# Kernel optimization log

Measured on AMD Instinct MI355X. Metric: run time of the kernel, lower is better.

Reference implementation:

```python
import jax, jax.numpy as jnp
import numpy as np

B, D, H, O = 4096, 1024, 8192, 1000

def _l2norm_rows(w):
    return w / jnp.maximum(jnp.linalg.norm(w, axis=1, keepdims=True), 1e-12)

def setup_inputs() -> dict:
    key = jax.random.key(0)
    k1, k2, k3 = jax.random.split(key, 3)
    x = jax.random.normal(k1, (B, D), dtype=jnp.float32)
    kohonen_weights = _l2norm_rows(jax.random.normal(k2, (H, D), dtype=jnp.float32))
    grossberg_weights = _l2norm_rows(jax.random.normal(k3, (O, H), dtype=jnp.float32))
    return {"x": x, "kohonen_weights": kohonen_weights, "grossberg_weights": grossberg_weights}

def reference(x, kohonen_weights, grossberg_weights):
    # x: [B, D] (already flat), kohonen_weights: [H, D], grossberg_weights: [O, H]
    x2 = jnp.sum(x * x, axis=1, keepdims=True)              # [B, 1]
    w2 = jnp.sum(kohonen_weights * kohonen_weights, axis=1)  # [H]
    # Euclidean cdist via the expanded quadratic form (same as torch.cdist p=2)
    sq = x2 + w2[None, :] - 2.0 * (x @ kohonen_weights.T)    # [B, H]
    distances = jnp.sqrt(jnp.maximum(sq, 0.0))
    winners = jnp.argmin(distances, axis=1)                  # [B] int
    # one_hot @ grossberg_weights.T is exactly a row gather of grossberg_weights.T
    output = jnp.take(grossberg_weights.T, winners, axis=0)  # [B, O]
    return (output, winners)
```

## Files before the change

kernel.cpp:

```cpp
#include <hip/hip_runtime.h>
#include <hip/hip_bf16.h>
#include <hip/hip_fp16.h>


#define BB 4096
#define DD 1024
#define HH 8192
#define OO 1000

#define BM 128
#define BN 128
#define BK 64
#define NTILES (HH / BN)

typedef _Float16 f16;
typedef _Float16 f16x4 __attribute__((ext_vector_type(4)));
typedef _Float16 f16x8 __attribute__((ext_vector_type(8)));
typedef float f32x4 __attribute__((ext_vector_type(4)));

typedef __attribute__((address_space(3))) uint32_t lds_u32_t;
typedef __attribute__((address_space(1))) uint32_t glb_u32_t;

__device__ __forceinline__ uint32_t packkey(float v, int col) {
  uint32_t u = __float_as_uint(v);
  uint32_t mask = (uint32_t)((int32_t)u >> 31) | 0x80000000u;
  u ^= mask;
  return (u & 0xFFFFFF80u) | (uint32_t)col;
}
__device__ __forceinline__ float unpackval(uint32_t k) {
  uint32_t u = k & 0xFFFFFF80u;
  uint32_t mask = (k & 0x80000000u) ? 0x80000000u : 0xFFFFFFFFu;
  return __uint_as_float(u ^ mask);
}

__device__ __forceinline__ void kmerge(uint32_t& k1, uint32_t& k2,
                                       uint32_t o1, uint32_t o2) {
  uint32_t mn = min(k1, o1);
  uint32_t alt = (k1 > o1) ? k2 : o2;
  k1 = max(k1, o1);
  k2 = max(mn, alt);
}

__global__ __launch_bounds__(256) void cvt_kernel(
    const float* __restrict__ x, const float* __restrict__ kw,
    f16* __restrict__ xh, f16* __restrict__ kh,
    const float* __restrict__ G, float* __restrict__ Gt) {
  const int blk = blockIdx.x;
  const int tid = threadIdx.x;
  __shared__ float tile[32][33];
  if (blk < BB + HH) {
    const float* src = (blk < BB) ? (x + (size_t)blk * DD)
                                  : (kw + (size_t)(blk - BB) * DD);
    f16* dst = (blk < BB) ? (xh + (size_t)blk * DD)
                          : (kh + (size_t)(blk - BB) * DD);
    float4 v = ((const float4*)src)[tid];
    f16x4 h;
    h[0] = (f16)v.x; h[1] = (f16)v.y; h[2] = (f16)v.z; h[3] = (f16)v.w;
    *(f16x4*)(dst + 4 * tid) = h;
  } else {
    const int tile_id = blk - (BB + HH);
    const int h0 = (tile_id >> 5) * 32;
    const int o0 = (tile_id & 31) * 32;
    const int tx = tid & 31;
    const int ty = tid >> 5;
#pragma unroll
    for (int j = 0; j < 4; ++j) {
      int o = o0 + ty + j * 8;
      if (o < OO) tile[ty + j * 8][tx] = G[(size_t)o * HH + h0 + tx];
    }
    __syncthreads();
#pragma unroll
    for (int j = 0; j < 4; ++j) {
      int o = o0 + tx;
      int h = h0 + ty + j * 8;
      if (o < OO) Gt[(size_t)h * OO + o] = tile[tx][ty + j * 8];
    }
  }
}

__global__ __launch_bounds__(256) void gemm_top2(
    const f16* __restrict__ A, const f16* __restrict__ Bt,
    uint2* __restrict__ pk) {
  __shared__ __align__(16) f16 sA[BM * BK];
  __shared__ __align__(16) f16 sB[BN * BK];
  __shared__ uint2 mk[128][2];

  const int tid = threadIdx.x;
  const int w = tid >> 6;
  const int L = tid & 63;
  const int m0 = blockIdx.y * BM;
  const int n0 = blockIdx.x * BN;
  const int rm = (w >> 1) * 64;
  const int cn = (w & 1) * 64;

  f32x4 acc[4][4];
#pragma unroll
  for (int i = 0; i < 4; ++i)
#pragma unroll
    for (int j = 0; j < 4; ++j) {
      acc[i][j][0] = 0.f; acc[i][j][1] = 0.f; acc[i][j][2] = 0.f; acc[i][j][3] = 0.f;
    }

  const int lm = L & 15;
  const int lq = L >> 4;

  const int r0 = tid >> 3;
  const int sc0 = ((tid & 7) ^ (r0 & 7)) * 8;
  const f16* pA = A + (size_t)(m0 + r0) * DD + sc0;
  const f16* pB = Bt + (size_t)(n0 + r0) * DD + sc0;
  const size_t rstep = (size_t)32 * DD;

  const int swz = (lm & 7);
  const int ra0 = (rm + lm) * BK + ((0 * 4 + lq) ^ swz) * 8;
  const int ra1 = (rm + lm) * BK + ((1 * 4 + lq) ^ swz) * 8;
  const int rb0 = (cn + lm) * BK + ((0 * 4 + lq) ^ swz) * 8;
  const int rb1 = (cn + lm) * BK + ((1 * 4 + lq) ^ swz) * 8;

  for (int kt = 0; kt < DD / BK; ++kt) {
    __syncthreads();
#pragma unroll
    for (int j = 0; j < 4; ++j) {
      __builtin_amdgcn_global_load_lds((const glb_u32_t*)(pA + j * rstep),
                                       (lds_u32_t*)(sA + (tid + j * 256) * 8), 16, 0, 0);
      __builtin_amdgcn_global_load_lds((const glb_u32_t*)(pB + j * rstep),
                                       (lds_u32_t*)(sB + (tid + j * 256) * 8), 16, 0, 0);
    }
    pA += BK; pB += BK;
    __syncthreads();

    f16x8 af[4], bf[4];
#pragma unroll
    for (int i = 0; i < 4; ++i)
      af[i] = *(const f16x8*)(sA + ra0 + i * 16 * BK);
#pragma unroll
    for (int j = 0; j < 4; ++j)
      bf[j] = *(const f16x8*)(sB + rb0 + j * 16 * BK);
#pragma unroll
    for (int i = 0; i < 4; ++i)
#pragma unroll
      for (int j = 0; j < 4; ++j)
        acc[i][j] = __builtin_amdgcn_mfma_f32_16x16x32_f16(af[i], bf[j], acc[i][j], 0, 0, 0);
#pragma unroll
    for (int i = 0; i < 4; ++i)
      af[i] = *(const f16x8*)(sA + ra1 + i * 16 * BK);
#pragma unroll
    for (int j = 0; j < 4; ++j)
      bf[j] = *(const f16x8*)(sB + rb1 + j * 16 * BK);
#pragma unroll
    for (int i = 0; i < 4; ++i)
#pragma unroll
      for (int j = 0; j < 4; ++j)
        acc[i][j] = __builtin_amdgcn_mfma_f32_16x16x32_f16(af[i], bf[j], acc[i][j], 0, 0, 0);
  }

  const int col0 = cn + lm;
#pragma unroll
  for (int i = 0; i < 4; ++i) {
#pragma unroll
    for (int r = 0; r < 4; ++r) {
      uint32_t k1 = 0, k2 = 0;
#pragma unroll
      for (int j = 0; j < 4; ++j) {
        uint32_t kj = packkey(acc[i][j][r], col0 + j * 16);
        if (kj > k1) { k2 = k1; k1 = kj; }
        else k2 = max(k2, kj);
      }
#pragma unroll
      for (int msk = 1; msk < 16; msk <<= 1) {
        uint32_t o1 = (uint32_t)__shfl_xor((int)k1, msk, 64);
        uint32_t o2 = (uint32_t)__shfl_xor((int)k2, msk, 64);
        kmerge(k1, k2, o1, o2);
      }
      if (lm == 0) {
        int rl = rm + i * 16 + lq * 4 + r;
        mk[rl][w & 1] = make_uint2(k1, k2);
      }
    }
  }
  __syncthreads();
  if (tid < 128) {
    uint2 a = mk[tid][0], b = mk[tid][1];
    kmerge(a.x, a.y, b.x, b.y);
    pk[(size_t)(m0 + tid) * NTILES + blockIdx.x] = a;
  }
}

__global__ __launch_bounds__(256) void select_kernel(
    const float* __restrict__ x, const float* __restrict__ kw,
    const uint2* __restrict__ pk,
    const float* __restrict__ Gt, float* __restrict__ out,
    float* __restrict__ out_w, int* __restrict__ winners) {
  const int b = blockIdx.x * 4 + (threadIdx.x >> 6);
  const int L = threadIdx.x & 63;

  const float4* x4 = (const float4*)(x + (size_t)b * DD);
  float4 xv[4];
#pragma unroll
  for (int j = 0; j < 4; ++j) xv[j] = x4[L + 64 * j];

  uint2 kp = pk[(size_t)b * NTILES + L];

  double x2 = 0.0;
#pragma unroll
  for (int j = 0; j < 4; ++j)
    x2 += (double)xv[j].x * xv[j].x + (double)xv[j].y * xv[j].y +
          (double)xv[j].z * xv[j].z + (double)xv[j].w * xv[j].w;
#pragma unroll
  for (int msk = 1; msk < 64; msk <<= 1) x2 += __shfl_xor(x2, msk, 64);

  uint32_t m = kp.x;
#pragma unroll
  for (int msk = 1; msk < 64; msk <<= 1)
    m = max(m, (uint32_t)__shfl_xor((int)m, msk, 64));
  const uint32_t thrk = packkey(unpackval(m) - 0.01f, 0);

  unsigned long long cand1 = __ballot(kp.x >= thrk);
  unsigned long long cand2 = __ballot(kp.y >= thrk);

  double best = 1e300;
  int bestc = 0x7fffffff;
#pragma unroll 1
  for (int pass = 0; pass < 2; ++pass) {
    unsigned long long bits = (pass == 0) ? cand1 : cand2;
    uint32_t mykey = (pass == 0) ? kp.x : kp.y;
    while (bits) {
      int t = __ffsll((long long)bits) - 1;
      bits &= bits - 1;
      uint32_t kbt = (uint32_t)__shfl((int)mykey, t, 64);
      int col = t * 128 + (int)(kbt & 127u);
      const float4* k4 = (const float4*)(kw + (size_t)col * DD);
      double dot = 0.0, w2 = 0.0;
#pragma unroll
      for (int j = 0; j < 4; ++j) {
        float4 wv = k4[L + 64 * j];
        dot += (double)xv[j].x * wv.x + (double)xv[j].y * wv.y +
               (double)xv[j].z * wv.z + (double)xv[j].w * wv.w;
        w2 += (double)wv.x * wv.x + (double)wv.y * wv.y +
              (double)wv.z * wv.z + (double)wv.w * wv.w;
      }
#pragma unroll
      for (int msk = 1; msk < 64; msk <<= 1) {
        dot += __shfl_xor(dot, msk, 64);
        w2 += __shfl_xor(w2, msk, 64);
      }
      double sq = x2 + w2 - 2.0 * dot;
      if (sq < best || (sq == best && col < bestc)) { best = sq; bestc = col; }
    }
  }

  if (L == 0) {
    out_w[b] = (float)bestc;
    winners[b] = bestc;
  }
  if (Gt != nullptr) {
    const float4* gsrc = (const float4*)(Gt + (size_t)bestc * OO);
    float4* gdst = (float4*)(out + (size_t)b * OO);
#pragma unroll
    for (int j = 0; j < 4; ++j) {
      int q = L + 64 * j;
      if (q < OO / 4) gdst[q] = gsrc[q];
    }
  }
}

__global__ __launch_bounds__(256) void gather_kernel(
    const float* __restrict__ G, const int* __restrict__ winners,
    float* __restrict__ out) {
  const int b = blockIdx.y;
  const int o = blockIdx.x * 256 + threadIdx.x;
  if (o < OO) {
    int w = winners[b];
    out[(size_t)b * OO + o] = G[(size_t)o * HH + w];
  }
}

extern "C" void kernel_launch(void* const* d_in, const int* in_sizes, int n_in,
                              void* d_out, int out_size, void* d_ws, size_t ws_size,
                              hipStream_t stream) {
  const float* x  = (const float*)d_in[0];
  const float* kw = (const float*)d_in[1];
  const float* gw = (const float*)d_in[2];
  float* out = (float*)d_out;

  const size_t MB = 1024 * 1024;
  char* ws = (char*)d_ws;
  f16*    xh      = (f16*)(ws);
  f16*    kh      = (f16*)(ws + 8 * MB);
  uint2*  pk      = (uint2*)(ws + 24 * MB);
  int*    winners = (int*)(ws + 26 * MB);
  float*  Gt      = (float*)(ws + 26 * MB + 65536);
  const size_t need = 26 * MB + 65536 + sizeof(float) * (size_t)HH * OO;
  const bool use_transpose = ws_size >= need;

  int cvt_blocks = BB + HH + (use_transpose ? 8192 : 0);
  cvt_kernel<<<cvt_blocks, 256, 0, stream>>>(x, kw, xh, kh, gw,
                                             use_transpose ? Gt : nullptr);

  dim3 g(HH / BN, BB / BM);
  gemm_top2<<<g, 256, 0, stream>>>(xh, kh, pk);

  select_kernel<<<BB / 4, 256, 0, stream>>>(x, kw, pk,
                                            use_transpose ? Gt : nullptr,
                                            out, out + (size_t)BB * OO, winners);

  if (!use_transpose) {
    gather_kernel<<<dim3((OO + 255) / 256, BB), 256, 0, stream>>>(gw, winners, out);
  }
}
```

Measured before the change: 226.0 us.

## Fuse convert, GEMM-top2 and select into one cooperative persistent kernel

Replaces the three separate launches (convert/transpose, GEMM with top-2 keys, select+gather) with a single cooperative kernel of 1024 persistent blocks that loops over the work and uses grid-wide syncs between phases. Each block handles two GEMM tiles and four select rows. The aim is to remove launch gaps and kernel boundary overheads. In exchange it adds grid.sync costs and caps occupancy at 4 blocks per CU. If the cooperative launch fails, it falls back to the multi-kernel path.

```diff
diff --git a/kernel.cpp b/kernel.cpp
--- a/kernel.cpp
+++ b/kernel.cpp
@@ -1,6 +1,9 @@
 #include <hip/hip_runtime.h>
 #include <hip/hip_bf16.h>
 #include <hip/hip_fp16.h>
+#include <hip/hip_cooperative_groups.h>
+
+namespace cg = cooperative_groups;
 
 
 #define BB 4096
@@ -12,6 +15,7 @@
 #define BN 128
 #define BK 64
 #define NTILES (HH / BN)
+#define GRID_BLKS 1024
 
 typedef _Float16 f16;
 typedef _Float16 f16x4 __attribute__((ext_vector_type(4)));
@@ -32,13 +36,270 @@
   uint32_t mask = (k & 0x80000000u) ? 0x80000000u : 0xFFFFFFFFu;
   return __uint_as_float(u ^ mask);
 }
-
 __device__ __forceinline__ void kmerge(uint32_t& k1, uint32_t& k2,
                                        uint32_t o1, uint32_t o2) {
   uint32_t mn = min(k1, o1);
   uint32_t alt = (k1 > o1) ? k2 : o2;
   k1 = max(k1, o1);
   k2 = max(mn, alt);
+}
+
+
+__device__ __forceinline__ void convert_row(const float* __restrict__ src,
+                                            f16* __restrict__ dst, int tid) {
+  float4 v = ((const float4*)src)[tid];
+  f16x4 h;
+  h[0] = (f16)v.x; h[1] = (f16)v.y; h[2] = (f16)v.z; h[3] = (f16)v.w;
+  *(f16x4*)(dst + 4 * tid) = h;
+}
+
+__device__ __forceinline__ void transpose_tile(const float* __restrict__ G,
+                                               float* __restrict__ Gt,
+                                               float (*tile)[33],
+                                               int tile_id, int tid) {
+  const int h0 = (tile_id >> 5) * 32;
+  const int o0 = (tile_id & 31) * 32;
+  const int tx = tid & 31;
+  const int ty = tid >> 5;
+  __syncthreads();
+#pragma unroll
+  for (int j = 0; j < 4; ++j) {
+    int o = o0 + ty + j * 8;
+    if (o < OO) tile[ty + j * 8][tx] = G[(size_t)o * HH + h0 + tx];
+  }
+  __syncthreads();
+#pragma unroll
+  for (int j = 0; j < 4; ++j) {
+    int o = o0 + tx;
+    int h = h0 + ty + j * 8;
+    if (o < OO) Gt[(size_t)h * OO + o] = tile[tx][ty + j * 8];
+  }
+}
+
+__device__ __forceinline__ void gemm_tile(const f16* __restrict__ A,
+                                          const f16* __restrict__ Bt,
+                                          uint2* __restrict__ pk,
+                                          f16* sA, f16* sB, uint2 (*mk)[2],
+                                          int bx, int by, int tid) {
+  const int w = tid >> 6;
+  const int L = tid & 63;
+  const int m0 = by * BM;
+  const int n0 = bx * BN;
+  const int rm = (w >> 1) * 64;
+  const int cn = (w & 1) * 64;
+
+  f32x4 acc[4][4];
+#pragma unroll
+  for (int i = 0; i < 4; ++i)
+#pragma unroll
+    for (int j = 0; j < 4; ++j) {
+      acc[i][j][0] = 0.f; acc[i][j][1] = 0.f; acc[i][j][2] = 0.f; acc[i][j][3] = 0.f;
+    }
+
+  const int lm = L & 15;
+  const int lq = L >> 4;
+
+  const int r0 = tid >> 3;
+  const int sc0 = ((tid & 7) ^ (r0 & 7)) * 8;
+  const f16* pA = A + (size_t)(m0 + r0) * DD + sc0;
+  const f16* pB = Bt + (size_t)(n0 + r0) * DD + sc0;
+  const size_t rstep = (size_t)32 * DD;
+
+  const int swz = (lm & 7);
+  const int ra0 = (rm + lm) * BK + ((0 * 4 + lq) ^ swz) * 8;
+  const int ra1 = (rm + lm) * BK + ((1 * 4 + lq) ^ swz) * 8;
+  const int rb0 = (cn + lm) * BK + ((0 * 4 + lq) ^ swz) * 8;
+  const int rb1 = (cn + lm) * BK + ((1 * 4 + lq) ^ swz) * 8;
+
+  for (int kt = 0; kt < DD / BK; ++kt) {
+    __syncthreads();
+#pragma unroll
+    for (int j = 0; j < 4; ++j) {
+      __builtin_amdgcn_global_load_lds((const glb_u32_t*)(pA + j * rstep),
+                                       (lds_u32_t*)(sA + (tid + j * 256) * 8), 16, 0, 0);
+      __builtin_amdgcn_global_load_lds((const glb_u32_t*)(pB + j * rstep),
+                                       (lds_u32_t*)(sB + (tid + j * 256) * 8), 16, 0, 0);
+    }
+    pA += BK; pB += BK;
+    __syncthreads();
+
+    f16x8 af[4], bf[4];
+#pragma unroll
+    for (int i = 0; i < 4; ++i)
+      af[i] = *(const f16x8*)(sA + ra0 + i * 16 * BK);
+#pragma unroll
+    for (int j = 0; j < 4; ++j)
+      bf[j] = *(const f16x8*)(sB + rb0 + j * 16 * BK);
+#pragma unroll
+    for (int i = 0; i < 4; ++i)
+#pragma unroll
+      for (int j = 0; j < 4; ++j)
+        acc[i][j] = __builtin_amdgcn_mfma_f32_16x16x32_f16(af[i], bf[j], acc[i][j], 0, 0, 0);
+#pragma unroll
+    for (int i = 0; i < 4; ++i)
+      af[i] = *(const f16x8*)(sA + ra1 + i * 16 * BK);
+#pragma unroll
+    for (int j = 0; j < 4; ++j)
+      bf[j] = *(const f16x8*)(sB + rb1 + j * 16 * BK);
+#pragma unroll
+    for (int i = 0; i < 4; ++i)
+#pragma unroll
+      for (int j = 0; j < 4; ++j)
+        acc[i][j] = __builtin_amdgcn_mfma_f32_16x16x32_f16(af[i], bf[j], acc[i][j], 0, 0, 0);
+  }
+
+  const int col0 = cn + lm;
+#pragma unroll
+  for (int i = 0; i < 4; ++i) {
+#pragma unroll
+    for (int r = 0; r < 4; ++r) {
+      uint32_t k1 = 0, k2 = 0;
+#pragma unroll
+      for (int j = 0; j < 4; ++j) {
+        uint32_t kj = packkey(acc[i][j][r], col0 + j * 16);
+        if (kj > k1) { k2 = k1; k1 = kj; }
+        else k2 = max(k2, kj);
+      }
+#pragma unroll
+      for (int msk = 1; msk < 16; msk <<= 1) {
+        uint32_t o1 = (uint32_t)__shfl_xor((int)k1, msk, 64);
+        uint32_t o2 = (uint32_t)__shfl_xor((int)k2, msk, 64);
+        kmerge(k1, k2, o1, o2);
+      }
+      if (lm == 0) {
+        int rl = rm + i * 16 + lq * 4 + r;
+        mk[rl][w & 1] = make_uint2(k1, k2);
+      }
+    }
+  }
+  __syncthreads();
+  if (tid < 128) {
+    uint2 a = mk[tid][0], b = mk[tid][1];
+    kmerge(a.x, a.y, b.x, b.y);
+    pk[(size_t)(m0 + tid) * NTILES + bx] = a;
+  }
+  __syncthreads();
+}
+
+__device__ __forceinline__ void select_row(const float* __restrict__ x,
+                                           const float* __restrict__ kw,
+                                           const uint2* __restrict__ pk,
+                                           const float* __restrict__ Gt,
+                                           const float* __restrict__ G,
+                                           float* __restrict__ out,
+                                           float* __restrict__ out_w,
+                                           int b, int L) {
+  const float4* x4 = (const float4*)(x + (size_t)b * DD);
+  float4 xv[4];
+#pragma unroll
+  for (int j = 0; j < 4; ++j) xv[j] = x4[L + 64 * j];
+
+  uint2 kp = pk[(size_t)b * NTILES + L];
+
+  double x2 = 0.0;
+#pragma unroll
+  for (int j = 0; j < 4; ++j)
+    x2 += (double)xv[j].x * xv[j].x + (double)xv[j].y * xv[j].y +
+          (double)xv[j].z * xv[j].z + (double)xv[j].w * xv[j].w;
+#pragma unroll
+  for (int msk = 1; msk < 64; msk <<= 1) x2 += __shfl_xor(x2, msk, 64);
+
+  uint32_t m = kp.x;
+#pragma unroll
+  for (int msk = 1; msk < 64; msk <<= 1)
+    m = max(m, (uint32_t)__shfl_xor((int)m, msk, 64));
+  const uint32_t thrk = packkey(unpackval(m) - 0.01f, 0);
+
+  unsigned long long cand1 = __ballot(kp.x >= thrk);
+  unsigned long long cand2 = __ballot(kp.y >= thrk);
+
+  double best = 1e300;
+  int bestc = 0x7fffffff;
+#pragma unroll 1
+  for (int pass = 0; pass < 2; ++pass) {
+    unsigned long long bits = (pass == 0) ? cand1 : cand2;
+    uint32_t mykey = (pass == 0) ? kp.x : kp.y;
+    while (bits) {
+      int t = __ffsll((long long)bits) - 1;
+      bits &= bits - 1;
+      uint32_t kbt = (uint32_t)__shfl((int)mykey, t, 64);
+      int col = t * 128 + (int)(kbt & 127u);
+      const float4* k4 = (const float4*)(kw + (size_t)col * DD);
+      double dot = 0.0, w2 = 0.0;
+#pragma unroll
+      for (int j = 0; j < 4; ++j) {
+        float4 wv = k4[L + 64 * j];
+        dot += (double)xv[j].x * wv.x + (double)xv[j].y * wv.y +
+               (double)xv[j].z * wv.z + (double)xv[j].w * wv.w;
+        w2 += (double)wv.x * wv.x + (double)wv.y * wv.y +
+              (double)wv.z * wv.z + (double)wv.w * wv.w;
+      }
+#pragma unroll
+      for (int msk = 1; msk < 64; msk <<= 1) {
+        dot += __shfl_xor(dot, msk, 64);
+        w2 += __shfl_xor(w2, msk, 64);
+      }
+      double sq = x2 + w2 - 2.0 * dot;
+      if (sq < best || (sq == best && col < bestc)) { best = sq; bestc = col; }
+    }
+  }
+
+  if (L == 0) out_w[b] = (float)bestc;
+  if (Gt != nullptr) {
+    const float4* gsrc = (const float4*)(Gt + (size_t)bestc * OO);
+    float4* gdst = (float4*)(out + (size_t)b * OO);
+#pragma unroll
+    for (int j = 0; j < 4; ++j) {
+      int q = L + 64 * j;
+      if (q < OO / 4) gdst[q] = gsrc[q];
+    }
+  } else {
+#pragma unroll 1
+    for (int j = 0; j < 16; ++j) {
+      int o = L + 64 * j;
+      if (o < OO) out[(size_t)b * OO + o] = G[(size_t)o * HH + bestc];
+    }
+  }
+}
+
+__global__ __launch_bounds__(256, 4) void mega_kernel(
+    const float* __restrict__ x, const float* __restrict__ kw,
+    const float* __restrict__ G,
+    f16* __restrict__ xh, f16* __restrict__ kh, float* __restrict__ Gt,
+    uint2* __restrict__ pk, float* __restrict__ out, float* __restrict__ out_w) {
+  __shared__ __align__(16) char smem[34816];
+  f16* sA = (f16*)smem;
+  f16* sB = (f16*)(smem + 16384);
+  uint2 (*mk)[2] = (uint2(*)[2])(smem + 32768);
+  float (*ttile)[33] = (float(*)[33])smem;
+
+  const int bid = blockIdx.x;
+  const int tid = threadIdx.x;
+  cg::grid_group grid = cg::this_grid();
+
+#pragma unroll 1
+  for (int r = bid; r < BB + HH; r += GRID_BLKS) {
+    const float* src = (r < BB) ? (x + (size_t)r * DD) : (kw + (size_t)(r - BB) * DD);
+    f16* dst = (r < BB) ? (xh + (size_t)r * DD) : (kh + (size_t)(r - BB) * DD);
+    convert_row(src, dst, tid);
+  }
+  if (Gt != nullptr) {
+#pragma unroll 1
+    for (int t = bid; t < 8192; t += GRID_BLKS)
+      transpose_tile(G, Gt, ttile, t, tid);
+  }
+  __threadfence();
+  grid.sync();
+
+#pragma unroll 1
+  for (int tt = 0; tt < 2; ++tt) {
+    int t = bid + tt * GRID_BLKS;
+    gemm_tile(xh, kh, pk, sA, sB, mk, t & 63, t >> 6, tid);
+  }
+  __threadfence();
+  grid.sync();
+
+  select_row(x, kw, pk, Gt, G, out, out_w, bid * 4 + (tid >> 6), tid & 63);
 }
 
 __global__ __launch_bounds__(256) void cvt_kernel(
@@ -53,28 +314,9 @@
                                   : (kw + (size_t)(blk - BB) * DD);
     f16* dst = (blk < BB) ? (xh + (size_t)blk * DD)
                           : (kh + (size_t)(blk - BB) * DD);
-    float4 v = ((const float4*)src)[tid];
-    f16x4 h;
-    h[0] = (f16)v.x; h[1] = (f16)v.y; h[2] = (f16)v.z; h[3] = (f16)v.w;
-    *(f16x4*)(dst + 4 * tid) = h;
+    convert_row(src, dst, tid);
   } else {
-    const int tile_id = blk - (BB + HH);
-    const int h0 = (tile_id >> 5) * 32;
-    const int o0 = (tile_id & 31) * 32;
-    const int tx = tid & 31;
-    const int ty = tid >> 5;
-#pragma unroll
-    for (int j = 0; j < 4; ++j) {
-      int o = o0 + ty + j * 8;
-      if (o < OO) tile[ty + j * 8][tx] = G[(size_t)o * HH + h0 + tx];
-    }
-    __syncthreads();
-#pragma unroll
-    for (int j = 0; j < 4; ++j) {
-      int o = o0 + tx;
-      int h = h0 + ty + j * 8;
-      if (o < OO) Gt[(size_t)h * OO + o] = tile[tx][ty + j * 8];
-    }
+    transpose_tile(G, Gt, tile, blk - (BB + HH), tid);
   }
 }
 
@@ -84,194 +326,16 @@
   __shared__ __align__(16) f16 sA[BM * BK];
   __shared__ __align__(16) f16 sB[BN * BK];
   __shared__ uint2 mk[128][2];
-
-  const int tid = threadIdx.x;
-  const int w = tid >> 6;
-  const int L = tid & 63;
-  const int m0 = blockIdx.y * BM;
-  const int n0 = blockIdx.x * BN;
-  const int rm = (w >> 1) * 64;
-  const int cn = (w & 1) * 64;
-
-  f32x4 acc[4][4];
-#pragma unroll
-  for (int i = 0; i < 4; ++i)
-#pragma unroll
-    for (int j = 0; j < 4; ++j) {
-      acc[i][j][0] = 0.f; acc[i][j][1] = 0.f; acc[i][j][2] = 0.f; acc[i][j][3] = 0.f;
-    }
-
-  const int lm = L & 15;
-  const int lq = L >> 4;
-
-  const int r0 = tid >> 3;
-  const int sc0 = ((tid & 7) ^ (r0 & 7)) * 8;
-  const f16* pA = A + (size_t)(m0 + r0) * DD + sc0;
-  const f16* pB = Bt + (size_t)(n0 + r0) * DD + sc0;
-  const size_t rstep = (size_t)32 * DD;
-
-  const int swz = (lm & 7);
-  const int ra0 = (rm + lm) * BK + ((0 * 4 + lq) ^ swz) * 8;
-  const int ra1 = (rm + lm) * BK + ((1 * 4 + lq) ^ swz) * 8;
-  const int rb0 = (cn + lm) * BK + ((0 * 4 + lq) ^ swz) * 8;
-  const int rb1 = (cn + lm) * BK + ((1 * 4 + lq) ^ swz) * 8;
-
-  for (int kt = 0; kt < DD / BK; ++kt) {
-    __syncthreads();
-#pragma unroll
-    for (int j = 0; j < 4; ++j) {
-      __builtin_amdgcn_global_load_lds((const glb_u32_t*)(pA + j * rstep),
-                                       (lds_u32_t*)(sA + (tid + j * 256) * 8), 16, 0, 0);
-      __builtin_amdgcn_global_load_lds((const glb_u32_t*)(pB + j * rstep),
-                                       (lds_u32_t*)(sB + (tid + j * 256) * 8), 16, 0, 0);
-    }
-    pA += BK; pB += BK;
-    __syncthreads();
-
-    f16x8 af[4], bf[4];
-#pragma unroll
-    for (int i = 0; i < 4; ++i)
-      af[i] = *(const f16x8*)(sA + ra0 + i * 16 * BK);
-#pragma unroll
-    for (int j = 0; j < 4; ++j)
-      bf[j] = *(const f16x8*)(sB + rb0 + j * 16 * BK);
-#pragma unroll
-    for (int i = 0; i < 4; ++i)
-#pragma unroll
-      for (int j = 0; j < 4; ++j)
-        acc[i][j] = __builtin_amdgcn_mfma_f32_16x16x32_f16(af[i], bf[j], acc[i][j], 0, 0, 0);
-#pragma unroll
-    for (int i = 0; i < 4; ++i)
-      af[i] = *(const f16x8*)(sA + ra1 + i * 16 * BK);
-#pragma unroll
-    for (int j = 0; j < 4; ++j)
-      bf[j] = *(const f16x8*)(sB + rb1 + j * 16 * BK);
-#pragma unroll
-    for (int i = 0; i < 4; ++i)
-#pragma unroll
-      for (int j = 0; j < 4; ++j)
-        acc[i][j] = __builtin_amdgcn_mfma_f32_16x16x32_f16(af[i], bf[j], acc[i][j], 0, 0, 0);
-  }
-
-  const int col0 = cn + lm;
-#pragma unroll
-  for (int i = 0; i < 4; ++i) {
-#pragma unroll
-    for (int r = 0; r < 4; ++r) {
-      uint32_t k1 = 0, k2 = 0;
-#pragma unroll
-      for (int j = 0; j < 4; ++j) {
-        uint32_t kj = packkey(acc[i][j][r], col0 + j * 16);
-        if (kj > k1) { k2 = k1; k1 = kj; }
-        else k2 = max(k2, kj);
-      }
-#pragma unroll
-      for (int msk = 1; msk < 16; msk <<= 1) {
-        uint32_t o1 = (uint32_t)__shfl_xor((int)k1, msk, 64);
-        uint32_t o2 = (uint32_t)__shfl_xor((int)k2, msk, 64);
-        kmerge(k1, k2, o1, o2);
-      }
-      if (lm == 0) {
-        int rl = rm + i * 16 + lq * 4 + r;
-        mk[rl][w & 1] = make_uint2(k1, k2);
-      }
-    }
-  }
-  __syncthreads();
-  if (tid < 128) {
-    uint2 a = mk[tid][0], b = mk[tid][1];
-    kmerge(a.x, a.y, b.x, b.y);
-    pk[(size_t)(m0 + tid) * NTILES + blockIdx.x] = a;
-  }
+  gemm_tile(A, Bt, pk, sA, sB, mk, blockIdx.x, blockIdx.y, threadIdx.x);
 }
 
 __global__ __launch_bounds__(256) void select_kernel(
     const float* __restrict__ x, const float* __restrict__ kw,
-    const uint2* __restrict__ pk,
-    const float* __restrict__ Gt, float* __restrict__ out,
-    float* __restrict__ out_w, int* __restrict__ winners) {
-  const int b = blockIdx.x * 4 + (threadIdx.x >> 6);
-  const int L = threadIdx.x & 63;
-
-  const float4* x4 = (const float4*)(x + (size_t)b * DD);
-  float4 xv[4];
-#pragma unroll
-  for (int j = 0; j < 4; ++j) xv[j] = x4[L + 64 * j];
-
-  uint2 kp = pk[(size_t)b * NTILES + L];
-
-  double x2 = 0.0;
-#pragma unroll
-  for (int j = 0; j < 4; ++j)
-    x2 += (double)xv[j].x * xv[j].x + (double)xv[j].y * xv[j].y +
-          (double)xv[j].z * xv[j].z + (double)xv[j].w * xv[j].w;
-#pragma unroll
-  for (int msk = 1; msk < 64; msk <<= 1) x2 += __shfl_xor(x2, msk, 64);
-
-  uint32_t m = kp.x;
-#pragma unroll
-  for (int msk = 1; msk < 64; msk <<= 1)
-    m = max(m, (uint32_t)__shfl_xor((int)m, msk, 64));
-  const uint32_t thrk = packkey(unpackval(m) - 0.01f, 0);
-
-  unsigned long long cand1 = __ballot(kp.x >= thrk);
-  unsigned long long cand2 = __ballot(kp.y >= thrk);
-
-  double best = 1e300;
-  int bestc = 0x7fffffff;
-#pragma unroll 1
-  for (int pass = 0; pass < 2; ++pass) {
-    unsigned long long bits = (pass == 0) ? cand1 : cand2;
-    uint32_t mykey = (pass == 0) ? kp.x : kp.y;
-    while (bits) {
-      int t = __ffsll((long long)bits) - 1;
-      bits &= bits - 1;
-      uint32_t kbt = (uint32_t)__shfl((int)mykey, t, 64);
-      int col = t * 128 + (int)(kbt & 127u);
-      const float4* k4 = (const float4*)(kw + (size_t)col * DD);
-      double dot = 0.0, w2 = 0.0;
-#pragma unroll
-      for (int j = 0; j < 4; ++j) {
-        float4 wv = k4[L + 64 * j];
-        dot += (double)xv[j].x * wv.x + (double)xv[j].y * wv.y +
-               (double)xv[j].z * wv.z + (double)xv[j].w * wv.w;
-        w2 += (double)wv.x * wv.x + (double)wv.y * wv.y +
-              (double)wv.z * wv.z + (double)wv.w * wv.w;
-      }
-#pragma unroll
-      for (int msk = 1; msk < 64; msk <<= 1) {
-        dot += __shfl_xor(dot, msk, 64);
-        w2 += __shfl_xor(w2, msk, 64);
-      }
-      double sq = x2 + w2 - 2.0 * dot;
-      if (sq < best || (sq == best && col < bestc)) { best = sq; bestc = col; }
-    }
-  }
-
-  if (L == 0) {
-    out_w[b] = (float)bestc;
-    winners[b] = bestc;
-  }
-  if (Gt != nullptr) {
-    const float4* gsrc = (const float4*)(Gt + (size_t)bestc * OO);
-    float4* gdst = (float4*)(out + (size_t)b * OO);
-#pragma unroll
-    for (int j = 0; j < 4; ++j) {
-      int q = L + 64 * j;
-      if (q < OO / 4) gdst[q] = gsrc[q];
-    }
-  }
-}
-
-__global__ __launch_bounds__(256) void gather_kernel(
-    const float* __restrict__ G, const int* __restrict__ winners,
-    float* __restrict__ out) {
-  const int b = blockIdx.y;
-  const int o = blockIdx.x * 256 + threadIdx.x;
-  if (o < OO) {
-    int w = winners[b];
-    out[(size_t)b * OO + o] = G[(size_t)o * HH + w];
-  }
+    const uint2* __restrict__ pk, const float* __restrict__ Gt,
+    const float* __restrict__ G, float* __restrict__ out,
+    float* __restrict__ out_w) {
+  select_row(x, kw, pk, Gt, G, out, out_w,
+             blockIdx.x * 4 + (threadIdx.x >> 6), threadIdx.x & 63);
 }
 
 extern "C" void kernel_launch(void* const* d_in, const int* in_sizes, int n_in,
@@ -281,29 +345,26 @@
   const float* kw = (const float*)d_in[1];
   const float* gw = (const float*)d_in[2];
   float* out = (float*)d_out;
+  float* out_w = out + (size_t)BB * OO;
 
   const size_t MB = 1024 * 1024;
   char* ws = (char*)d_ws;
-  f16*    xh      = (f16*)(ws);
-  f16*    kh      = (f16*)(ws + 8 * MB);
-  uint2*  pk      = (uint2*)(ws + 24 * MB);
-  int*    winners = (int*)(ws + 26 * MB);
-  float*  Gt      = (float*)(ws + 26 * MB + 65536);
+  f16*    xh = (f16*)(ws);
+  f16*    kh = (f16*)(ws + 8 * MB);
+  uint2*  pk = (uint2*)(ws + 24 * MB);
+  float*  Gt = (float*)(ws + 26 * MB + 65536);
   const size_t need = 26 * MB + 65536 + sizeof(float) * (size_t)HH * OO;
-  const bool use_transpose = ws_size >= need;
-
-  int cvt_blocks = BB + HH + (use_transpose ? 8192 : 0);
-  cvt_kernel<<<cvt_blocks, 256, 0, stream>>>(x, kw, xh, kh, gw,
-                                             use_transpose ? Gt : nullptr);
-
-  dim3 g(HH / BN, BB / BM);
-  gemm_top2<<<g, 256, 0, stream>>>(xh, kh, pk);
-
-  select_kernel<<<BB / 4, 256, 0, stream>>>(x, kw, pk,
-                                            use_transpose ? Gt : nullptr,
-                                            out, out + (size_t)BB * OO, winners);
-
-  if (!use_transpose) {
-    gather_kernel<<<dim3((OO + 255) / 256, BB), 256, 0, stream>>>(gw, winners, out);
-  }
-}
+  float* GtArg = (ws_size >= need) ? Gt : nullptr;
+
+  void* kargs[] = {(void*)&x, (void*)&kw, (void*)&gw, (void*)&xh, (void*)&kh,
+                   (void*)&GtArg, (void*)&pk, (void*)&out, (void*)&out_w};
+  hipError_t e = hipLaunchCooperativeKernel((void*)mega_kernel, dim3(GRID_BLKS),
+                                            dim3(256), kargs, 0, stream);
+  if (e != hipSuccess) {
+    int cvt_blocks = BB + HH + (GtArg ? 8192 : 0);
+    cvt_kernel<<<cvt_blocks, 256, 0, stream>>>(x, kw, xh, kh, gw, GtArg);
+    dim3 g(HH / BN, BB / BM);
+    gemm_top2<<<g, 256, 0, stream>>>(xh, kh, pk);
+    select_kernel<<<BB / 4, 256, 0, stream>>>(x, kw, pk, GtArg, gw, out, out_w);
+  }
+}
```

After: 684.5 us. 203% more time.

## Move Grossberg transpose into GEMM launch and fold fallback gather into select

Applied to the files above, without the earlier changes.

The G transpose work moves out of the conversion kernel and into extra blocks appended to the GEMM grid, so it overlaps with the matmul tiles instead of delaying them. The conversion kernel now handles four rows per block, and the fallback gather is merged into the select kernel, which drops the separate winners buffer and the extra launch. The transpose blocks reuse the GEMM's shared memory and take up slots on the GPU alongside the matmul blocks. Whether the transpose finishes before the select kernel needs it now depends on how the GEMM launch schedules its blocks.

```diff
diff --git a/kernel.cpp b/kernel.cpp
--- a/kernel.cpp
+++ b/kernel.cpp
@@ -32,7 +32,6 @@
   uint32_t mask = (k & 0x80000000u) ? 0x80000000u : 0xFFFFFFFFu;
   return __uint_as_float(u ^ mask);
 }
-
 __device__ __forceinline__ void kmerge(uint32_t& k1, uint32_t& k2,
                                        uint32_t o1, uint32_t o2) {
   uint32_t mn = min(k1, o1);
@@ -43,53 +42,64 @@
 
 __global__ __launch_bounds__(256) void cvt_kernel(
     const float* __restrict__ x, const float* __restrict__ kw,
-    f16* __restrict__ xh, f16* __restrict__ kh,
-    const float* __restrict__ G, float* __restrict__ Gt) {
-  const int blk = blockIdx.x;
+    f16* __restrict__ xh, f16* __restrict__ kh) {
   const int tid = threadIdx.x;
-  __shared__ float tile[32][33];
-  if (blk < BB + HH) {
-    const float* src = (blk < BB) ? (x + (size_t)blk * DD)
-                                  : (kw + (size_t)(blk - BB) * DD);
-    f16* dst = (blk < BB) ? (xh + (size_t)blk * DD)
-                          : (kh + (size_t)(blk - BB) * DD);
+#pragma unroll
+  for (int i = 0; i < 4; ++i) {
+    int r = blockIdx.x * 4 + i;
+    const float* src = (r < BB) ? (x + (size_t)r * DD)
+                                : (kw + (size_t)(r - BB) * DD);
+    f16* dst = (r < BB) ? (xh + (size_t)r * DD)
+                        : (kh + (size_t)(r - BB) * DD);
     float4 v = ((const float4*)src)[tid];
     f16x4 h;
     h[0] = (f16)v.x; h[1] = (f16)v.y; h[2] = (f16)v.z; h[3] = (f16)v.w;
     *(f16x4*)(dst + 4 * tid) = h;
-  } else {
-    const int tile_id = blk - (BB + HH);
-    const int h0 = (tile_id >> 5) * 32;
-    const int o0 = (tile_id & 31) * 32;
-    const int tx = tid & 31;
-    const int ty = tid >> 5;
-#pragma unroll
-    for (int j = 0; j < 4; ++j) {
-      int o = o0 + ty + j * 8;
-      if (o < OO) tile[ty + j * 8][tx] = G[(size_t)o * HH + h0 + tx];
-    }
-    __syncthreads();
-#pragma unroll
-    for (int j = 0; j < 4; ++j) {
-      int o = o0 + tx;
-      int h = h0 + ty + j * 8;
-      if (o < OO) Gt[(size_t)h * OO + o] = tile[tx][ty + j * 8];
-    }
   }
 }
 
 __global__ __launch_bounds__(256) void gemm_top2(
     const f16* __restrict__ A, const f16* __restrict__ Bt,
-    uint2* __restrict__ pk) {
+    uint2* __restrict__ pk,
+    const float* __restrict__ G, float* __restrict__ Gt) {
   __shared__ __align__(16) f16 sA[BM * BK];
   __shared__ __align__(16) f16 sB[BN * BK];
   __shared__ uint2 mk[128][2];
 
   const int tid = threadIdx.x;
+  const int t = blockIdx.x;
+
+  if (t >= 2048) {
+    if (Gt == nullptr) return;
+    float (*tile)[33] = (float(*)[33])sA;
+    const int tx = tid & 31;
+    const int ty = tid >> 5;
+#pragma unroll 1
+    for (int j4 = 0; j4 < 4; ++j4) {
+      int tile_id = (t - 2048) * 4 + j4;
+      int h0 = (tile_id >> 5) * 32;
+      int o0 = (tile_id & 31) * 32;
+      __syncthreads();
+#pragma unroll
+      for (int j = 0; j < 4; ++j) {
+        int o = o0 + ty + j * 8;
+        if (o < OO) tile[ty + j * 8][tx] = G[(size_t)o * HH + h0 + tx];
+      }
+      __syncthreads();
+#pragma unroll
+      for (int j = 0; j < 4; ++j) {
+        int o = o0 + tx;
+        int h = h0 + ty + j * 8;
+        if (o < OO) Gt[(size_t)h * OO + o] = tile[tx][ty + j * 8];
+      }
+    }
+    return;
+  }
+
   const int w = tid >> 6;
   const int L = tid & 63;
-  const int m0 = blockIdx.y * BM;
-  const int n0 = blockIdx.x * BN;
+  const int m0 = (t >> 6) * BM;
+  const int n0 = (t & 63) * BN;
   const int rm = (w >> 1) * 64;
   const int cn = (w & 1) * 64;
 
@@ -181,15 +191,15 @@
   if (tid < 128) {
     uint2 a = mk[tid][0], b = mk[tid][1];
     kmerge(a.x, a.y, b.x, b.y);
-    pk[(size_t)(m0 + tid) * NTILES + blockIdx.x] = a;
+    pk[(size_t)(m0 + tid) * NTILES + (t & 63)] = a;
   }
 }
 
 __global__ __launch_bounds__(256) void select_kernel(
     const float* __restrict__ x, const float* __restrict__ kw,
     const uint2* __restrict__ pk,
-    const float* __restrict__ Gt, float* __restrict__ out,
-    float* __restrict__ out_w, int* __restrict__ winners) {
+    const float* __restrict__ Gt, const float* __restrict__ G,
+    float* __restrict__ out, float* __restrict__ out_w) {
   const int b = blockIdx.x * 4 + (threadIdx.x >> 6);
   const int L = threadIdx.x & 63;
 
@@ -224,10 +234,10 @@
     unsigned long long bits = (pass == 0) ? cand1 : cand2;
     uint32_t mykey = (pass == 0) ? kp.x : kp.y;
     while (bits) {
-      int t = __ffsll((long long)bits) - 1;
+      int tt = __ffsll((long long)bits) - 1;
       bits &= bits - 1;
-      uint32_t kbt = (uint32_t)__shfl((int)mykey, t, 64);
-      int col = t * 128 + (int)(kbt & 127u);
+      uint32_t kbt = (uint32_t)__shfl((int)mykey, tt, 64);
+      int col = tt * 128 + (int)(kbt & 127u);
       const float4* k4 = (const float4*)(kw + (size_t)col * DD);
       double dot = 0.0, w2 = 0.0;
 #pragma unroll
@@ -248,10 +258,7 @@
     }
   }
 
-  if (L == 0) {
-    out_w[b] = (float)bestc;
-    winners[b] = bestc;
-  }
+  if (L == 0) out_w[b] = (float)bestc;
   if (Gt != nullptr) {
     const float4* gsrc = (const float4*)(Gt + (size_t)bestc * OO);
     float4* gdst = (float4*)(out + (size_t)b * OO);
@@ -260,17 +267,12 @@
       int q = L + 64 * j;
       if (q < OO / 4) gdst[q] = gsrc[q];
     }
-  }
-}
-
-__global__ __launch_bounds__(256) void gather_kernel(
-    const float* __restrict__ G, const int* __restrict__ winners,
-    float* __restrict__ out) {
-  const int b = blockIdx.y;
-  const int o = blockIdx.x * 256 + threadIdx.x;
-  if (o < OO) {
-    int w = winners[b];
-    out[(size_t)b * OO + o] = G[(size_t)o * HH + w];
+  } else {
+#pragma unroll 1
+    for (int j = 0; j < 16; ++j) {
+      int o = L + 64 * j;
+      if (o < OO) out[(size_t)b * OO + o] = G[(size_t)o * HH + bestc];
+    }
   }
 }
 
@@ -281,29 +283,21 @@
   const float* kw = (const float*)d_in[1];
   const float* gw = (const float*)d_in[2];
   float* out = (float*)d_out;
+  float* out_w = out + (size_t)BB * OO;
 
   const size_t MB = 1024 * 1024;
   char* ws = (char*)d_ws;
-  f16*    xh      = (f16*)(ws);
-  f16*    kh      = (f16*)(ws + 8 * MB);
-  uint2*  pk      = (uint2*)(ws + 24 * MB);
-  int*    winners = (int*)(ws + 26 * MB);
-  float*  Gt      = (float*)(ws + 26 * MB + 65536);
+  f16*    xh = (f16*)(ws);
+  f16*    kh = (f16*)(ws + 8 * MB);
+  uint2*  pk = (uint2*)(ws + 24 * MB);
+  float*  Gt = (float*)(ws + 26 * MB + 65536);
   const size_t need = 26 * MB + 65536 + sizeof(float) * (size_t)HH * OO;
-  const bool use_transpose = ws_size >= need;
-
-  int cvt_blocks = BB + HH + (use_transpose ? 8192 : 0);
-  cvt_kernel<<<cvt_blocks, 256, 0, stream>>>(x, kw, xh, kh, gw,
-                                             use_transpose ? Gt : nullptr);
-
-  dim3 g(HH / BN, BB / BM);
-  gemm_top2<<<g, 256, 0, stream>>>(xh, kh, pk);
-
-  select_kernel<<<BB / 4, 256, 0, stream>>>(x, kw, pk,
-                                            use_transpose ? Gt : nullptr,
-                                            out, out + (size_t)BB * OO, winners);
-
-  if (!use_transpose) {
-    gather_kernel<<<dim3((OO + 255) / 256, BB), 256, 0, stream>>>(gw, winners, out);
-  }
-}
+  float* GtArg = (ws_size >= need) ? Gt : nullptr;
+
+  cvt_kernel<<<(BB + HH) / 4, 256, 0, stream>>>(x, kw, xh, kh);
+
+  int gemm_blocks = 2048 + (GtArg ? 2048 : 0);
+  gemm_top2<<<gemm_blocks, 256, 0, stream>>>(xh, kh, pk, gw, GtArg);
+
+  select_kernel<<<BB / 4, 256, 0, stream>>>(x, kw, pk, GtArg, gw, out, out_w);
+}
```

Result: slower. 252.4 us (+11.7%).
